# Performance work log

Measured on AMD Instinct MI355X. Metric: run time of the kernel, lower is better.

Reference implementation:

```python
import jax, jax.numpy as jnp
import numpy as np

B, S, H, EMB, VOCAB, LABEL, NUM_LAYERS = 32, 512, 256, 256, 32000, 16, 3


def _before(x):  # shift right along seq dim, zero-pad front
    z = jnp.zeros_like(x[:, :1])
    return jnp.concatenate([z, x[:, :-1]], axis=1)


def _after(x):  # shift left along seq dim, zero-pad end
    z = jnp.zeros_like(x[:, :1])
    return jnp.concatenate([x[:, 1:], z], axis=1)


def setup_inputs() -> dict:
    key = jax.random.key(0)
    ks = jax.random.split(key, 12)
    p = lambda k, shape: (0.02 * jax.random.normal(k, shape)).astype(jnp.float32)
    return {
        "span_nodes": jnp.zeros((1,), jnp.int32),
        "bert_vec": jnp.zeros((1,), jnp.float32),
        "node_text": jax.random.randint(ks[0], (B, S), 0, VOCAB),
        "word_mask": jnp.ones((B, S), jnp.float32),
        "sent_mask": jnp.ones((1,), jnp.int32),
        "node_feature": jnp.zeros((1,), jnp.float32),
        "adj": jnp.zeros((1,), jnp.int32),
        # embedding + emb_proj
        "E": p(ks[1], (VOCAB, EMB)),
        "Wp": p(ks[2], (EMB, H)), "bp": jnp.zeros((H,), jnp.float32),
        # SCell: W(3H->7H, no bias), U(emb->7H, no bias), V(H->7H, bias)
        "Ws": p(ks[3], (3 * H, 7 * H)), "Us": p(ks[4], (EMB, 7 * H)),
        "Vs": p(ks[5], (H, 7 * H)), "bVs": jnp.zeros((7 * H,), jnp.float32),
        # GCell: W(H->2H, no bias), w(H->H, no bias), U(H->2H, bias), u(H->H, bias)
        "WgW": p(ks[6], (H, 2 * H)), "Wgw": p(ks[7], (H, H)),
        "UgU": p(ks[8], (H, 2 * H)), "bgU": jnp.zeros((2 * H,), jnp.float32),
        "ugu": p(ks[9], (H, H)), "bgu": jnp.zeros((H,), jnp.float32),
        # output head
        "Wo": p(ks[10], (H, LABEL)), "bo": jnp.zeros((LABEL,), jnp.float32),
    }


def _slstm(node_text, word_mask, E, Wp, bp, Ws, Us, Vs, bVs,
           WgW, Wgw, UgU, bgU, ugu, bgu, Wo, bo):
    mask = word_mask[..., None]                      # [B,S,1]
    emb = E[node_text]                               # [B,S,EMB]
    proj = (emb @ Wp + bp) * mask                    # [B,S,H] (dropout=identity in eval)
    h = proj
    c = proj
    g = h.mean(1)                                    # [B,H]
    c_g = c.mean(1)                                  # [B,H]
    xU = emb @ Us                                    # [B,S,7H] hoisted (constant per layer)
    neg = ((1.0 - word_mask) * 1e16)[..., None]      # [B,S,1]
    for _ in range(NUM_LAYERS):
        h = h * mask
        c = c * mask
        # SCell
        hcat = jnp.concatenate([_before(h), h, _after(h)], axis=-1)   # [B,S,3H]
        gates = hcat @ Ws + xU + (g @ Vs + bVs)[:, None, :]           # [B,S,7H]
        gi, gl, gr, gf, gs, go, gu = jnp.split(gates, 7, axis=-1)
        gu = jnp.tanh(gu)
        # sigmoid then softmax over the stacked-gate dim (note: o stays raw, as in source)
        stk = jax.nn.softmax(jax.nn.sigmoid(jnp.stack([gi, gl, gr, gf, gs], axis=-2)), axis=-2)
        gi, gl, gr, gf, gs = (stk[..., k, :] for k in range(5))
        new_c = _before(c) * gl + c * gf + gr * _after(c) + gs * c_g[:, None, :] + gi * gu
        new_h = go * jnp.tanh(new_c)
        # GCell (uses pre-update h, c)
        h_avg = h.mean(1)                                             # [B,H]
        fo = jax.nn.sigmoid(g @ WgW + h_avg @ UgU + bgU)              # [B,2H]
        f_g, o_g = jnp.split(fo, 2, axis=-1)
        f_w = jax.nn.sigmoid((g @ Wgw)[:, None, :] + h @ ugu + bgu) - neg   # [B,S,H]
        f_w = jax.nn.softmax(f_w, axis=1)
        new_c_g = f_g * c_g + (c * f_w).sum(1)
        new_g = o_g * jnp.tanh(new_c_g)
        h, c, g, c_g = new_h, new_c, new_g, new_c_g
    return (g @ Wo + bo, g.mean(0) @ Wo + bo)


def reference(span_nodes, bert_vec, node_text, word_mask, sent_mask, node_feature, adj,
              E, Wp, bp, Ws, Us, Vs, bVs, WgW, Wgw, UgU, bgU, ugu, bgu, Wo, bo):
    return _slstm(node_text, word_mask, E, Wp, bp, Ws, Us, Vs, bVs,
                  WgW, Wgw, UgU, bgU, ugu, bgu, Wo, bo)
```

## Files before the change

kernel.cpp:

```cpp
#include <hip/hip_runtime.h>
#include <math.h>

#define B_      32
#define S_      512
#define H_      256
#define EMB_    256
#define M_      (B_*S_)
#define N7_     1792
#define NG_     2048
#define NS_     2560
#define KA_     1024
#define LABEL_  16

#define BM 128
#define BN 256
#define BK 32
#define EBM 64

typedef __bf16 bf16x8 __attribute__((ext_vector_type(8)));
typedef float  f32x4  __attribute__((ext_vector_type(4)));

__device__ __forceinline__ float sigf(float x){ return 1.f/(1.f+__expf(-x)); }

__device__ __forceinline__ unsigned short f2bf(float f){
    union { float f; unsigned int u; } v; v.f = f;
    unsigned int r = v.u + 0x7FFFu + ((v.u >> 16) & 1u);
    return (unsigned short)(r >> 16);
}
__device__ __forceinline__ float bf2f(unsigned short u){
    union { unsigned int i; float f; } v; v.i = ((unsigned int)u) << 16; return v.f;
}

__global__ void prep_waugT(const float* __restrict__ Ws, const float* __restrict__ Us,
                           const float* __restrict__ ugu, unsigned short* __restrict__ WaugT,
                           unsigned short* __restrict__ zpage){
    if(blockIdx.x == 0) zpage[threadIdx.x] = 0;
    long idx = (long)blockIdx.x*256 + threadIdx.x;
    int j = (int)(idx >> 10), k = (int)(idx & 1023);
    int tg = j >> 7, rem = j & 127, p = rem >> 4, t = tg*16 + (rem & 15);
    float v = 0.f;
    if(p < 7){
        int col = p*256 + t;
        v = (k < 768) ? Ws[(long)k*N7_ + col] : Us[(long)(k-768)*N7_ + col];
    } else if(k >= 256 && k < 512){
        v = ugu[(k-256)*H_ + t];
    }
    WaugT[idx] = f2bf(v);
}

__global__ void prep_wpT(const float* __restrict__ Wp, unsigned short* __restrict__ WpT){
    int idx = blockIdx.x*256 + threadIdx.x;
    int j = idx >> 8, k = idx & 255;
    WpT[idx] = f2bf(Wp[k*H_ + j]);
}

__global__ void emb_cast(const int* __restrict__ idx, const float* __restrict__ E,
                         unsigned short* __restrict__ embbf){
    int i = blockIdx.x, t = threadIdx.x;
    embbf[(size_t)i*EMB_ + t] = f2bf(E[(size_t)idx[i]*EMB_ + t]);
}

__global__ __launch_bounds__(256, 2) void embed_mfma(
        const unsigned short* __restrict__ embbf, const unsigned short* __restrict__ WpT,
        const float* __restrict__ bp, const float* __restrict__ mask,
        unsigned short* __restrict__ h0b, float* __restrict__ c0){
    __shared__ unsigned short As[2][EBM*BK];
    __shared__ unsigned short Bs[2][H_*BK];
    int tid = threadIdx.x, w = tid>>6, l = tid&63, fr = l&15, fq = l>>4;
    int m0 = blockIdx.x * EBM;
    f32x4 acc[4][4];
    #pragma unroll
    for(int m=0;m<4;m++)
        #pragma unroll
        for(int n=0;n<4;n++) acc[m][n] = (f32x4){0.f,0.f,0.f,0.f};

    auto stage = [&](int buf, int kt){
        {
            int row = tid >> 2;
            int k0 = ((tid & 3) ^ ((row >> 1) & 3)) * 8;
            const unsigned short* src = embbf + (size_t)(m0+row)*EMB_ + kt + k0;
            __builtin_amdgcn_global_load_lds(
                (const __attribute__((address_space(1))) unsigned int*)src,
                (__attribute__((address_space(3))) unsigned int*)(&As[buf][w*512]),
                16, 0, 0);
        }
        #pragma unroll
        for(int q=0;q<4;q++){
            int v = q*256 + tid;
            int col = v >> 2;
            int k0 = ((v & 3) ^ ((col >> 1) & 3)) * 8;
            const unsigned short* src = WpT + (size_t)col*EMB_ + kt + k0;
            __builtin_amdgcn_global_load_lds(
                (const __attribute__((address_space(1))) unsigned int*)src,
                (__attribute__((address_space(3))) unsigned int*)(&Bs[buf][(q*256 + w*64)*8]),
                16, 0, 0);
        }
    };

    stage(0, 0);
    __syncthreads();
    int cur = 0;
    for(int step=0; step<EMB_/BK; step++){
        if(step+1 < EMB_/BK) stage(cur^1, (step+1)*BK);
        bf16x8 bfv[4];
        #pragma unroll
        for(int n=0;n<4;n++){
            int colr = w*64 + n*16 + fr;
            int slot = fq ^ ((colr >> 1) & 3);
            bfv[n] = *(const bf16x8*)(&Bs[cur][colr*BK + slot*8]);
        }
        #pragma unroll
        for(int m=0;m<4;m++){
            int rowr = m*16 + fr;
            int slot = fq ^ ((rowr >> 1) & 3);
            bf16x8 af = *(const bf16x8*)(&As[cur][rowr*BK + slot*8]);
            #pragma unroll
            for(int n=0;n<4;n++)
                acc[m][n] = __builtin_amdgcn_mfma_f32_16x16x32_bf16(af, bfv[n], acc[m][n], 0,0,0);
        }
        __syncthreads();
        cur ^= 1;
    }
    #pragma unroll
    for(int m=0;m<4;m++){
        #pragma unroll
        for(int j=0;j<4;j++){
            int i = m0 + m*16 + fq*4 + j;
            float mk = mask[i];
            #pragma unroll
            for(int n=0;n<4;n++){
                int col = w*64 + n*16 + fr;
                float v = (acc[m][n][j] + bp[col]) * mk;
                h0b[(size_t)i*H_ + col] = f2bf(v);
                c0 [(size_t)i*H_ + col] = v;
            }
        }
    }
}

__global__ void reduce_mean_s(const unsigned short* __restrict__ h, float* __restrict__ outA,
                              float* __restrict__ outB){
    __shared__ float part[4][256];
    int b = blockIdx.x;
    int hh = threadIdx.x & 255, sg = threadIdx.x >> 8;
    float s = 0.f;
    long base = ((long)b*S_ + sg*128)*H_ + hh;
    for(int ss=0; ss<128; ss++) s += bf2f(h[base + (long)ss*H_]);
    part[sg][hh] = s;
    __syncthreads();
    if(threadIdx.x < 256){
        float t = (part[0][hh]+part[1][hh]+part[2][hh]+part[3][hh]) * (1.f/S_);
        outA[b*H_+hh] = t;
        if(outB) outB[b*H_+hh] = t;
    }
}

__global__ void small_gemm(const float* __restrict__ g, const float* __restrict__ havg,
                           const float* __restrict__ Vs, const float* __restrict__ bVs,
                           const float* __restrict__ Wgw, const float* __restrict__ bgu,
                           const float* __restrict__ WgW, const float* __restrict__ UgU,
                           const float* __restrict__ bgU, float* __restrict__ smalls){
    __shared__ float gs[256], hs[256];
    int b = blockIdx.y, t0 = threadIdx.x;
    gs[t0] = g[b*H_+t0];
    hs[t0] = havg[b*H_+t0];
    __syncthreads();
    int j = blockIdx.x*256 + t0;
    float acc;
    if(j < NG_){
        int tg = j >> 7, rem = j & 127, p = rem >> 4, t = tg*16 + (rem & 15);
        if(p < 7){
            int col = p*256 + t;
            acc = bVs[col];
            for(int k=0;k<H_;k++) acc += gs[k]*Vs[k*N7_+col];
        } else {
            acc = bgu[t];
            for(int k=0;k<H_;k++) acc += gs[k]*Wgw[k*H_+t];
        }
    } else {
        int jj = j - NG_;
        acc = bgU[jj];
        for(int k=0;k<H_;k++) acc += gs[k]*WgW[k*512+jj] + hs[k]*UgU[k*512+jj];
        acc = sigf(acc);
    }
    smalls[b*NS_+j] = acc;
}

__global__ __launch_bounds__(256, 2) void layer_mfma(
        const unsigned short* __restrict__ hbf, const unsigned short* __restrict__ embbf,
        const unsigned short* __restrict__ WaugT, const unsigned short* __restrict__ zpage,
        const float* __restrict__ c_old, const float* __restrict__ cg_old,
        const float* __restrict__ smalls, const float* __restrict__ mask,
        unsigned short* __restrict__ hbf_new, float* __restrict__ c_new,
        float* __restrict__ lpart, float* __restrict__ apart, float* __restrict__ hpart){
    __shared__ unsigned short As[2][BM*BK];
    __shared__ unsigned short Bs[2][BN*BK];
    __shared__ float red[4][16][3];
    int tid = threadIdx.x;
    int w = tid >> 6, l = tid & 63;
    int fr = l & 15, fq = l >> 4;
    int wr = w >> 1, wc = w & 1;
    int n0 = blockIdx.x * BN;
    int m0 = blockIdx.y * BM;
    int b  = m0 >> 9;

    f32x4 acc[4][8];
    #pragma unroll
    for(int m=0;m<4;m++)
        #pragma unroll
        for(int n=0;n<8;n++) acc[m][n] = (f32x4){0.f,0.f,0.f,0.f};

    auto stage = [&](int buf, int kt){
        int region = kt >> 8;
        #pragma unroll
        for(int q=0;q<2;q++){
            int u = q*256 + tid;
            int row = u >> 2;
            int k0 = ((u & 3) ^ ((row >> 1) & 3)) * 8;
            const unsigned short* src;
            if(region < 3){
                int i  = m0 + row;
                int si = (i & (S_-1)) + region - 1;
                src = ((unsigned)si < (unsigned)S_)
                    ? hbf + (size_t)(i + region - 1)*H_ + (kt & 255) + k0
                    : zpage + k0;
            } else {
                src = embbf + (size_t)(m0 + row)*EMB_ + (kt - 768) + k0;
            }
            __builtin_amdgcn_global_load_lds(
                (const __attribute__((address_space(1))) unsigned int*)src,
                (__attribute__((address_space(3))) unsigned int*)(&As[buf][(q*256 + w*64)*8]),
                16, 0, 0);
        }
        #pragma unroll
        for(int q=0;q<4;q++){
            int v = q*256 + tid;
            int col = v >> 2;
            int k0 = ((v & 3) ^ ((col >> 1) & 3)) * 8;
            const unsigned short* src = WaugT + (size_t)(n0 + col)*KA_ + kt + k0;
            __builtin_amdgcn_global_load_lds(
                (const __attribute__((address_space(1))) unsigned int*)src,
                (__attribute__((address_space(3))) unsigned int*)(&Bs[buf][(q*256 + w*64)*8]),
                16, 0, 0);
        }
    };

    stage(0, 0);
    __syncthreads();
    int cur = 0;
    for(int step=0; step<KA_/BK; step++){
        if(step+1 < KA_/BK) stage(cur^1, (step+1)*BK);
        bf16x8 bfv[8];
        #pragma unroll
        for(int n=0;n<8;n++){
            int colr = wc*128 + n*16 + fr;
            int slot = fq ^ ((colr >> 1) & 3);
            bfv[n] = *(const bf16x8*)(&Bs[cur][colr*BK + slot*8]);
        }
        #pragma unroll
        for(int m=0;m<4;m++){
            int rowr = wr*64 + m*16 + fr;
            int slot = fq ^ ((rowr >> 1) & 3);
            bf16x8 af = *(const bf16x8*)(&As[cur][rowr*BK + slot*8]);
            #pragma unroll
            for(int n=0;n<8;n++)
                acc[m][n] = __builtin_amdgcn_mfma_f32_16x16x32_bf16(af, bfv[n], acc[m][n], 0,0,0);
        }
        __syncthreads();
        cur ^= 1;
    }

    int t = (n0 >> 3) + wc*16 + fr;
    float sm[8];
    #pragma unroll
    for(int n=0;n<8;n++) sm[n] = smalls[b*NS_ + n0 + wc*128 + n*16 + fr];
    float cgv = cg_old[b*H_ + t];
    float lsum = 0.f, asum = 0.f, hsum = 0.f;
    #pragma unroll
    for(int m=0;m<4;m++){
        #pragma unroll
        for(int j=0;j<4;j++){
            int i = m0 + wr*64 + m*16 + fq*4 + j;
            int s = i & (S_-1);
            float gv[8];
            #pragma unroll
            for(int n=0;n<8;n++) gv[n] = acc[m][n][j] + sm[n];
            float ei=__expf(sigf(gv[0])), el=__expf(sigf(gv[1])), er=__expf(sigf(gv[2]));
            float ef=__expf(sigf(gv[3])), es=__expf(sigf(gv[4]));
            float inv = 1.f/(ei+el+er+ef+es);
            float c0v = c_old[(size_t)i*H_ + t];
            float cbv = (s>0)      ? c_old[(size_t)(i-1)*H_ + t] : 0.f;
            float cav = (s<S_-1)   ? c_old[(size_t)(i+1)*H_ + t] : 0.f;
            float tu = tanhf(gv[6]);
            float nc = (cbv*el + c0v*ef + er*cav + es*cgv + ei*tu)*inv;
            float nh = gv[5]*tanhf(nc);
            float mk = mask[i];
            float ncm = nc*mk, nhm = nh*mk;
            c_new [(size_t)i*H_ + t] = ncm;
            hbf_new[(size_t)i*H_ + t] = f2bf(nhm);
            float e = __expf(sigf(gv[7]) - (1.f - mk)*1e16f);
            lsum += e;
            asum += e*c0v;
            hsum += nhm;
        }
    }
    #pragma unroll
    for(int off=16; off<64; off<<=1){
        lsum += __shfl_xor(lsum, off);
        asum += __shfl_xor(asum, off);
        hsum += __shfl_xor(hsum, off);
    }
    if(l < 16){ red[w][l][0]=lsum; red[w][l][1]=asum; red[w][l][2]=hsum; }
    __syncthreads();
    if(tid < 32){
        int wc2 = tid >> 4, fr2 = tid & 15;
        float L  = red[wc2][fr2][0] + red[2+wc2][fr2][0];
        float A  = red[wc2][fr2][1] + red[2+wc2][fr2][1];
        float Hh = red[wc2][fr2][2] + red[2+wc2][fr2][2];
        int tt = (n0 >> 3) + wc2*16 + fr2;
        int by = blockIdx.y;
        lpart[by*H_ + tt] = L;
        apart[by*H_ + tt] = A;
        hpart[by*H_ + tt] = Hh;
    }
}

__global__ void gcell2x(const float* __restrict__ lpart, const float* __restrict__ apart,
                        const float* __restrict__ hpart, const float* __restrict__ cg_old,
                        const float* __restrict__ smalls,
                        float* __restrict__ g_new, float* __restrict__ cg_new,
                        float* __restrict__ havg_out){
    int b = blockIdx.x, t = threadIdx.x;
    float L = 0.f, A = 0.f, Hs = 0.f;
    for(int ci=0; ci<4; ci++){
        int by = b*4 + ci;
        L  += lpart[by*H_ + t];
        A  += apart[by*H_ + t];
        Hs += hpart[by*H_ + t];
    }
    float fg = smalls[b*NS_ + NG_ + t];
    float og = smalls[b*NS_ + NG_ + 256 + t];
    float ncg = fg*cg_old[b*H_+t] + A/L;
    g_new[b*H_+t]    = og*tanhf(ncg);
    cg_new[b*H_+t]   = ncg;
    havg_out[b*H_+t] = Hs * (1.f/S_);
}

__global__ void outk(const float* __restrict__ g, const float* __restrict__ Wo,
                     const float* __restrict__ bo, float* __restrict__ out){
    __shared__ float o1[B_*LABEL_];
    int t = threadIdx.x;
    if(t < B_*LABEL_){
        int b = t/LABEL_, j = t%LABEL_;
        float acc = bo[j];
        for(int k=0;k<H_;k++) acc += g[b*H_+k]*Wo[k*LABEL_+j];
        o1[t] = acc;
        out[t] = acc;
    }
    __syncthreads();
    if(t < LABEL_){
        float s = 0.f;
        for(int b=0;b<B_;b++) s += o1[b*LABEL_+t];
        out[B_*LABEL_+t] = s*(1.f/B_);
    }
}

extern "C" void kernel_launch(void* const* d_in, const int* in_sizes, int n_in,
                              void* d_out, int out_size, void* d_ws, size_t ws_size,
                              hipStream_t stream){
    const int*   node_text = (const int*)  d_in[2];
    const float* word_mask = (const float*)d_in[3];
    const float* E   = (const float*)d_in[7];
    const float* Wp  = (const float*)d_in[8];
    const float* bp  = (const float*)d_in[9];
    const float* Ws  = (const float*)d_in[10];
    const float* Us  = (const float*)d_in[11];
    const float* Vs  = (const float*)d_in[12];
    const float* bVs = (const float*)d_in[13];
    const float* WgW = (const float*)d_in[14];
    const float* Wgw = (const float*)d_in[15];
    const float* UgU = (const float*)d_in[16];
    const float* bgU = (const float*)d_in[17];
    const float* ugu = (const float*)d_in[18];
    const float* bgu = (const float*)d_in[19];
    const float* Wo  = (const float*)d_in[20];
    const float* bo  = (const float*)d_in[21];

    float* w = (float*)d_ws;
    size_t off = 0;
    auto alloc = [&](size_t nfloats){ float* p = w + off; off += nfloats; return p; };
    unsigned short* WaugT = (unsigned short*)alloc((size_t)NG_*KA_/2);
    unsigned short* zpage = (unsigned short*)alloc(128);
    unsigned short* WpT   = (unsigned short*)alloc((size_t)H_*EMB_/2);
    unsigned short* embbf = (unsigned short*)alloc((size_t)M_*EMB_/2);
    unsigned short* hbf[2] = { (unsigned short*)alloc((size_t)M_*H_/2),
                               (unsigned short*)alloc((size_t)M_*H_/2) };
    float* cb[2]  = { alloc((size_t)M_*H_), alloc((size_t)M_*H_) };
    float* lpart  = alloc((size_t)(M_/BM)*H_);
    float* apart  = alloc((size_t)(M_/BM)*H_);
    float* hpart  = alloc((size_t)(M_/BM)*H_);
    float* gb[2]  = { alloc(B_*H_), alloc(B_*H_) };
    float* cgb[2] = { alloc(B_*H_), alloc(B_*H_) };
    float* havg   = alloc(B_*H_);
    float* smalls = alloc((size_t)B_*NS_);

    prep_waugT<<<(NG_*KA_)/256, 256, 0, stream>>>(Ws, Us, ugu, WaugT, zpage);
    prep_wpT<<<(H_*EMB_)/256, 256, 0, stream>>>(Wp, WpT);
    emb_cast<<<M_, 256, 0, stream>>>(node_text, E, embbf);
    embed_mfma<<<M_/EBM, 256, 0, stream>>>(embbf, WpT, bp, word_mask, hbf[0], cb[0]);
    reduce_mean_s<<<B_, 1024, 0, stream>>>(hbf[0], gb[0], cgb[0]);

    int cur = 0;
    for(int layer=0; layer<3; layer++){
        int nxt = cur ^ 1;
        const float* havg_in = (layer == 0) ? gb[0] : havg;
        small_gemm<<<dim3(NS_/256, B_), 256, 0, stream>>>(gb[cur], havg_in, Vs, bVs,
                                                          Wgw, bgu, WgW, UgU, bgU, smalls);
        layer_mfma<<<dim3(NG_/BN, M_/BM), 256, 0, stream>>>(hbf[cur], embbf, WaugT, zpage,
                                                            cb[cur], cgb[cur], smalls, word_mask,
                                                            hbf[nxt], cb[nxt],
                                                            lpart, apart, hpart);
        gcell2x<<<B_, 256, 0, stream>>>(lpart, apart, hpart, cgb[cur], smalls,
                                        gb[nxt], cgb[nxt], havg);
        cur = nxt;
    }
    outk<<<1, 512, 0, stream>>>(gb[cur], Wo, bo, (float*)d_out);
}
```

Baseline: 400.6 us.

## Triple-buffer LDS staging in layer GEMM with partial vmcnt waits and setprio

Moves the layer MFMA kernel's K-loop from double to triple buffering. Two tiles are kept in flight, and the wait uses an explicit s_waitcnt vmcnt(12) so only the oldest tile's loads must finish before the barrier. The MFMA block is also wrapped in s_setprio to favour matrix issue. This raises LDS use by half, which with launch_bounds(256,2) may limit occupancy, and it relies on a hand-counted vmcnt that matches the 12 loads per stage.

```diff
diff --git a/kernel.cpp b/kernel.cpp
--- a/kernel.cpp
+++ b/kernel.cpp
@@ -15,6 +15,7 @@
 #define BM 128
 #define BN 256
 #define BK 32
+#define NSTEP (KA_/BK)
 #define EBM 64
 
 typedef __bf16 bf16x8 __attribute__((ext_vector_type(8)));
@@ -193,8 +194,8 @@
         const float* __restrict__ smalls, const float* __restrict__ mask,
         unsigned short* __restrict__ hbf_new, float* __restrict__ c_new,
         float* __restrict__ lpart, float* __restrict__ apart, float* __restrict__ hpart){
-    __shared__ unsigned short As[2][BM*BK];
-    __shared__ unsigned short Bs[2][BN*BK];
+    __shared__ unsigned short As[3][BM*BK];
+    __shared__ unsigned short Bs[3][BN*BK];
     __shared__ float red[4][16][3];
     int tid = threadIdx.x;
     int w = tid >> 6, l = tid & 63;
@@ -245,29 +246,54 @@
         }
     };
 
-    stage(0, 0);
-    __syncthreads();
-    int cur = 0;
-    for(int step=0; step<KA_/BK; step++){
-        if(step+1 < KA_/BK) stage(cur^1, (step+1)*BK);
+    auto compute = [&](int c){
         bf16x8 bfv[8];
         #pragma unroll
         for(int n=0;n<8;n++){
             int colr = wc*128 + n*16 + fr;
             int slot = fq ^ ((colr >> 1) & 3);
-            bfv[n] = *(const bf16x8*)(&Bs[cur][colr*BK + slot*8]);
-        }
+            bfv[n] = *(const bf16x8*)(&Bs[c][colr*BK + slot*8]);
+        }
+        bf16x8 afv[4];
         #pragma unroll
         for(int m=0;m<4;m++){
             int rowr = wr*64 + m*16 + fr;
             int slot = fq ^ ((rowr >> 1) & 3);
-            bf16x8 af = *(const bf16x8*)(&As[cur][rowr*BK + slot*8]);
+            afv[m] = *(const bf16x8*)(&As[c][rowr*BK + slot*8]);
+        }
+        __builtin_amdgcn_s_setprio(1);
+        #pragma unroll
+        for(int m=0;m<4;m++)
             #pragma unroll
             for(int n=0;n<8;n++)
-                acc[m][n] = __builtin_amdgcn_mfma_f32_16x16x32_bf16(af, bfv[n], acc[m][n], 0,0,0);
-        }
-        __syncthreads();
-        cur ^= 1;
+                acc[m][n] = __builtin_amdgcn_mfma_f32_16x16x32_bf16(afv[m], bfv[n], acc[m][n], 0,0,0);
+        __builtin_amdgcn_s_setprio(0);
+    };
+
+    stage(0, 0);
+    stage(1, BK);
+    int cur = 0;
+    #pragma unroll 1
+    for(int step=0; step<NSTEP-2; ++step){
+        int tb = cur + 2; if(tb >= 3) tb -= 3;
+        stage(tb, (step+2)*BK);
+        asm volatile("s_waitcnt vmcnt(12)" ::: "memory");
+        __builtin_amdgcn_s_barrier();
+        asm volatile("" ::: "memory");
+        compute(cur);
+        asm volatile("" ::: "memory");
+        __builtin_amdgcn_s_barrier();
+        cur = cur + 1; if(cur >= 3) cur -= 3;
+    }
+    #pragma unroll 1
+    for(int rem=0; rem<2; ++rem){
+        asm volatile("s_waitcnt vmcnt(0)" ::: "memory");
+        __builtin_amdgcn_s_barrier();
+        asm volatile("" ::: "memory");
+        compute(cur);
+        asm volatile("" ::: "memory");
+        __builtin_amdgcn_s_barrier();
+        cur = cur + 1; if(cur >= 3) cur -= 3;
     }
 
     int t = (n0 >> 3) + wc*16 + fr;
```

Result: slower. 410.9 us (+2.6%).

## Enlarge layer GEMM tile to 256x256x64 with 8 waves and interleaved staging

Applied to the files above, without the earlier changes.

The main per-layer MFMA GEMM moves from 128x256 tiles with BK=32 and 4 waves to 256x256 tiles with BK=64 and 8 waves. The next k-tile's loads are split into four quarter-stages interleaved with the MFMA sub-steps, using explicit vmcnt waits, raw barriers and setprio around the MFMA clusters. The LDS swizzle is widened to 8 slots. This aims to raise arithmetic intensity and hide global-to-LDS latency, at the cost of much more LDS per block (128 KB for double buffering), which may limit occupancy and halves the number of blocks. The embed kernel is hardcoded to its old 32 k-step, and the partial reductions are adjusted for two row blocks per batch.

```diff
diff --git a/kernel.cpp b/kernel.cpp
--- a/kernel.cpp
+++ b/kernel.cpp
@@ -12,9 +12,10 @@
 #define KA_     1024
 #define LABEL_  16
 
-#define BM 128
+#define BM 256
 #define BN 256
-#define BK 32
+#define BK 64
+#define NT (KA_/BK)
 #define EBM 64
 
 typedef __bf16 bf16x8 __attribute__((ext_vector_type(8)));
@@ -64,8 +65,8 @@
         const unsigned short* __restrict__ embbf, const unsigned short* __restrict__ WpT,
         const float* __restrict__ bp, const float* __restrict__ mask,
         unsigned short* __restrict__ h0b, float* __restrict__ c0){
-    __shared__ unsigned short As[2][EBM*BK];
-    __shared__ unsigned short Bs[2][H_*BK];
+    __shared__ unsigned short As[2][EBM*32];
+    __shared__ unsigned short Bs[2][H_*32];
     int tid = threadIdx.x, w = tid>>6, l = tid&63, fr = l&15, fq = l>>4;
     int m0 = blockIdx.x * EBM;
     f32x4 acc[4][4];
@@ -100,20 +101,20 @@
     stage(0, 0);
     __syncthreads();
     int cur = 0;
-    for(int step=0; step<EMB_/BK; step++){
-        if(step+1 < EMB_/BK) stage(cur^1, (step+1)*BK);
+    for(int step=0; step<EMB_/32; step++){
+        if(step+1 < EMB_/32) stage(cur^1, (step+1)*32);
         bf16x8 bfv[4];
         #pragma unroll
         for(int n=0;n<4;n++){
             int colr = w*64 + n*16 + fr;
             int slot = fq ^ ((colr >> 1) & 3);
-            bfv[n] = *(const bf16x8*)(&Bs[cur][colr*BK + slot*8]);
+            bfv[n] = *(const bf16x8*)(&Bs[cur][colr*32 + slot*8]);
         }
         #pragma unroll
         for(int m=0;m<4;m++){
             int rowr = m*16 + fr;
             int slot = fq ^ ((rowr >> 1) & 3);
-            bf16x8 af = *(const bf16x8*)(&As[cur][rowr*BK + slot*8]);
+            bf16x8 af = *(const bf16x8*)(&As[cur][rowr*32 + slot*8]);
             #pragma unroll
             for(int n=0;n<4;n++)
                 acc[m][n] = __builtin_amdgcn_mfma_f32_16x16x32_bf16(af, bfv[n], acc[m][n], 0,0,0);
@@ -186,7 +187,7 @@
     smalls[b*NS_+j] = acc;
 }
 
-__global__ __launch_bounds__(256, 2) void layer_mfma(
+__global__ __launch_bounds__(512, 2) void layer_mfma(
         const unsigned short* __restrict__ hbf, const unsigned short* __restrict__ embbf,
         const unsigned short* __restrict__ WaugT, const unsigned short* __restrict__ zpage,
         const float* __restrict__ c_old, const float* __restrict__ cg_old,
@@ -195,11 +196,11 @@
         float* __restrict__ lpart, float* __restrict__ apart, float* __restrict__ hpart){
     __shared__ unsigned short As[2][BM*BK];
     __shared__ unsigned short Bs[2][BN*BK];
-    __shared__ float red[4][16][3];
+    __shared__ float red[8][16][3];
     int tid = threadIdx.x;
     int w = tid >> 6, l = tid & 63;
     int fr = l & 15, fq = l >> 4;
-    int wr = w >> 1, wc = w & 1;
+    int wr = w >> 1, wcl = w & 1;
     int n0 = blockIdx.x * BN;
     int m0 = blockIdx.y * BM;
     int b  = m0 >> 9;
@@ -210,70 +211,97 @@
         #pragma unroll
         for(int n=0;n<8;n++) acc[m][n] = (f32x4){0.f,0.f,0.f,0.f};
 
-    auto stage = [&](int buf, int kt){
-        int region = kt >> 8;
-        #pragma unroll
-        for(int q=0;q<2;q++){
-            int u = q*256 + tid;
-            int row = u >> 2;
-            int k0 = ((u & 3) ^ ((row >> 1) & 3)) * 8;
-            const unsigned short* src;
-            if(region < 3){
-                int i  = m0 + row;
-                int si = (i & (S_-1)) + region - 1;
-                src = ((unsigned)si < (unsigned)S_)
-                    ? hbf + (size_t)(i + region - 1)*H_ + (kt & 255) + k0
-                    : zpage + k0;
-            } else {
-                src = embbf + (size_t)(m0 + row)*EMB_ + (kt - 768) + k0;
+    auto stage_half = [&](int buf, int kt, int p){
+        if(p < 2){
+            int region = kt >> 8;
+            #pragma unroll
+            for(int q=0;q<2;q++){
+                int u   = q*512 + tid;
+                int row = p*128 + (u >> 3);
+                int k0  = ((u & 7) ^ (row & 7)) * 8;
+                const unsigned short* src;
+                if(region < 3){
+                    int i  = m0 + row;
+                    int si = (i & (S_-1)) + region - 1;
+                    src = ((unsigned)si < (unsigned)S_)
+                        ? hbf + (size_t)(i + region - 1)*H_ + (kt & 255) + k0
+                        : zpage + k0;
+                } else {
+                    src = embbf + (size_t)(m0 + row)*EMB_ + (kt - 768) + k0;
+                }
+                __builtin_amdgcn_global_load_lds(
+                    (const __attribute__((address_space(1))) unsigned int*)src,
+                    (__attribute__((address_space(3))) unsigned int*)
+                        (&As[buf][p*8192 + (q*512 + w*64)*8]),
+                    16, 0, 0);
             }
-            __builtin_amdgcn_global_load_lds(
-                (const __attribute__((address_space(1))) unsigned int*)src,
-                (__attribute__((address_space(3))) unsigned int*)(&As[buf][(q*256 + w*64)*8]),
-                16, 0, 0);
-        }
-        #pragma unroll
-        for(int q=0;q<4;q++){
-            int v = q*256 + tid;
-            int col = v >> 2;
-            int k0 = ((v & 3) ^ ((col >> 1) & 3)) * 8;
-            const unsigned short* src = WaugT + (size_t)(n0 + col)*KA_ + kt + k0;
-            __builtin_amdgcn_global_load_lds(
-                (const __attribute__((address_space(1))) unsigned int*)src,
-                (__attribute__((address_space(3))) unsigned int*)(&Bs[buf][(q*256 + w*64)*8]),
-                16, 0, 0);
+        } else {
+            int hf = p - 2;
+            #pragma unroll
+            for(int q=0;q<2;q++){
+                int u   = q*512 + tid;
+                int col = hf*128 + (u >> 3);
+                int k0  = ((u & 7) ^ (col & 7)) * 8;
+                const unsigned short* src = WaugT + (size_t)(n0 + col)*KA_ + kt + k0;
+                __builtin_amdgcn_global_load_lds(
+                    (const __attribute__((address_space(1))) unsigned int*)src,
+                    (__attribute__((address_space(3))) unsigned int*)
+                        (&Bs[buf][hf*8192 + (q*512 + w*64)*8]),
+                    16, 0, 0);
+            }
         }
     };
 
-    stage(0, 0);
-    __syncthreads();
-    int cur = 0;
-    for(int step=0; step<KA_/BK; step++){
-        if(step+1 < KA_/BK) stage(cur^1, (step+1)*BK);
-        bf16x8 bfv[8];
-        #pragma unroll
-        for(int n=0;n<8;n++){
-            int colr = wc*128 + n*16 + fr;
-            int slot = fq ^ ((colr >> 1) & 3);
-            bfv[n] = *(const bf16x8*)(&Bs[cur][colr*BK + slot*8]);
-        }
-        #pragma unroll
-        for(int m=0;m<4;m++){
-            int rowr = wr*64 + m*16 + fr;
-            int slot = fq ^ ((rowr >> 1) & 3);
-            bf16x8 af = *(const bf16x8*)(&As[cur][rowr*BK + slot*8]);
-            #pragma unroll
-            for(int n=0;n<8;n++)
-                acc[m][n] = __builtin_amdgcn_mfma_f32_16x16x32_bf16(af, bfv[n], acc[m][n], 0,0,0);
-        }
-        __syncthreads();
-        cur ^= 1;
-    }
-
-    int t = (n0 >> 3) + wc*16 + fr;
+    #pragma unroll
+    for(int p=0;p<4;p++) stage_half(0, 0, p);
+
+    bf16x8 afv[4];
+    #pragma unroll 1
+    for(int t=0; t<NT; ++t){
+        int buf = t & 1;
+        int kt  = t * BK;
+        if(t+1 < NT){
+            stage_half(buf^1, kt+BK, 0);
+            asm volatile("s_waitcnt vmcnt(2)" ::: "memory");
+        } else {
+            asm volatile("s_waitcnt vmcnt(0)" ::: "memory");
+        }
+        __builtin_amdgcn_s_barrier();
+        #pragma unroll
+        for(int p=0;p<4;p++){
+            if(p && t+1 < NT) stage_half(buf^1, kt+BK, p);
+            int ks = p >> 1, nh = p & 1;
+            if(nh == 0){
+                #pragma unroll
+                for(int m=0;m<4;m++){
+                    int row  = wr*64 + m*16 + fr;
+                    int slot = (ks*4 + fq) ^ (row & 7);
+                    afv[m] = *(const bf16x8*)(&As[buf][row*BK + slot*8]);
+                }
+            }
+            bf16x8 bfv[4];
+            #pragma unroll
+            for(int nn=0;nn<4;nn++){
+                int col  = wcl*128 + (nh*4+nn)*16 + fr;
+                int slot = (ks*4 + fq) ^ (col & 7);
+                bfv[nn] = *(const bf16x8*)(&Bs[buf][col*BK + slot*8]);
+            }
+            __builtin_amdgcn_s_setprio(1);
+            #pragma unroll
+            for(int m=0;m<4;m++)
+                #pragma unroll
+                for(int nn=0;nn<4;nn++)
+                    acc[m][nh*4+nn] = __builtin_amdgcn_mfma_f32_16x16x32_bf16(
+                                          afv[m], bfv[nn], acc[m][nh*4+nn], 0,0,0);
+            __builtin_amdgcn_s_setprio(0);
+        }
+        __builtin_amdgcn_s_barrier();
+    }
+
+    int t = (n0 >> 3) + wcl*16 + fr;
     float sm[8];
     #pragma unroll
-    for(int n=0;n<8;n++) sm[n] = smalls[b*NS_ + n0 + wc*128 + n*16 + fr];
+    for(int n=0;n<8;n++) sm[n] = smalls[b*NS_ + n0 + wcl*128 + n*16 + fr];
     float cgv = cg_old[b*H_ + t];
     float lsum = 0.f, asum = 0.f, hsum = 0.f;
     #pragma unroll
@@ -314,9 +342,13 @@
     __syncthreads();
     if(tid < 32){
         int wc2 = tid >> 4, fr2 = tid & 15;
-        float L  = red[wc2][fr2][0] + red[2+wc2][fr2][0];
-        float A  = red[wc2][fr2][1] + red[2+wc2][fr2][1];
-        float Hh = red[wc2][fr2][2] + red[2+wc2][fr2][2];
+        float L = 0.f, A = 0.f, Hh = 0.f;
+        #pragma unroll
+        for(int k=0;k<4;k++){
+            L  += red[2*k + wc2][fr2][0];
+            A  += red[2*k + wc2][fr2][1];
+            Hh += red[2*k + wc2][fr2][2];
+        }
         int tt = (n0 >> 3) + wc2*16 + fr2;
         int by = blockIdx.y;
         lpart[by*H_ + tt] = L;
@@ -332,8 +364,8 @@
                         float* __restrict__ havg_out){
     int b = blockIdx.x, t = threadIdx.x;
     float L = 0.f, A = 0.f, Hs = 0.f;
-    for(int ci=0; ci<4; ci++){
-        int by = b*4 + ci;
+    for(int ci=0; ci<2; ci++){
+        int by = b*2 + ci;
         L  += lpart[by*H_ + t];
         A  += apart[by*H_ + t];
         Hs += hpart[by*H_ + t];
@@ -416,7 +448,7 @@
         const float* havg_in = (layer == 0) ? gb[0] : havg;
         small_gemm<<<dim3(NS_/256, B_), 256, 0, stream>>>(gb[cur], havg_in, Vs, bVs,
                                                           Wgw, bgu, WgW, UgU, bgU, smalls);
-        layer_mfma<<<dim3(NG_/BN, M_/BM), 256, 0, stream>>>(hbf[cur], embbf, WaugT, zpage,
+        layer_mfma<<<dim3(NG_/BN, M_/BM), 512, 0, stream>>>(hbf[cur], embbf, WaugT, zpage,
                                                             cb[cur], cgb[cur], smalls, word_mask,
                                                             hbf[nxt], cb[nxt],
                                                             lpart, apart, hpart);
```

Measured after the change: 414.5 us. +3.5%, slower.
